# Kernel tuning notes

Measured on AMD Instinct MI355X. Metric: run time of the kernel, lower is better.

## Reference

```python
import jax, jax.numpy as jnp
import numpy as np

EPS = 1e-08
DIM = 256


def setup_inputs() -> dict:
    key = jax.random.key(0)
    k1, k2, k3 = jax.random.split(key, 3)
    B, S, D = 4, 4096, DIM
    x = jax.random.normal(k1, (B, S, D), dtype=jnp.float32)
    mask = jnp.ones((B, S), dtype=bool)
    # params of nn.Linear(dim, dim) and log_temp = log(0.1)
    bound = 1.0 / np.sqrt(D)
    W_v = jax.random.uniform(k2, (D, D), minval=-bound, maxval=bound, dtype=jnp.float32)
    b_v = jax.random.uniform(k3, (D,), minval=-bound, maxval=bound, dtype=jnp.float32)
    log_temp = jnp.log(jnp.asarray(0.1, dtype=jnp.float32))
    return {"x": x, "W_v": W_v, "b_v": b_v, "log_temp": log_temp, "mask": mask}


def reference(x, W_v, b_v, log_temp, mask):
    # temperature = exp(log_temp).clamp_min(1e-5)
    temp = jnp.maximum(jnp.exp(log_temp), 1e-5).astype(x.dtype)
    # squared pairwise euclidean distances (cdist^2), clamped to >= 0
    sq = jnp.sum(x * x, axis=-1)  # [B, S]
    d2 = sq[:, :, None] + sq[:, None, :] - 2.0 * jnp.einsum('bsd,btd->bst', x, x)
    d2 = jnp.maximum(d2, 0.0)  # [B, S, S]
    # Cauchy kernel: 1 / (1 + (dist/temp)^2)
    kernel = 1.0 / (1.0 + d2 / (temp * temp))
    valid = (mask[:, None, :] & mask[:, :, None]).astype(kernel.dtype)
    kernel = kernel * valid
    # row-normalize
    attn = kernel / jnp.maximum(jnp.sum(kernel, axis=-1, keepdims=True), EPS)
    v = x @ W_v.T + b_v  # [B, S, D]
    out = jnp.einsum('bst,btd->bsd', attn, v)
    return out
```

## Files before the change

### kernel.cpp

```cpp
#include <hip/hip_runtime.h>
#include <hip/hip_bf16.h>

#define S 4096
#define D 256
#define NB 4

typedef __attribute__((ext_vector_type(8))) __bf16 bf16x8;
typedef __attribute__((ext_vector_type(8))) short s16x8;
typedef __attribute__((ext_vector_type(4))) short s16x4;
typedef __attribute__((ext_vector_type(4))) float f32x4;
typedef __attribute__((ext_vector_type(8))) _Float16 h16x8;

#define MFMA(a, b, c) __builtin_amdgcn_mfma_f32_16x16x32_bf16(a, b, c, 0, 0, 0)
#define MFMA8(a, b, c) __builtin_amdgcn_mfma_f32_16x16x32_fp8_fp8(a, b, c, 0, 0, 0)

__device__ __forceinline__ short f2bf(float f) {
    union { float f; unsigned u; } v; v.f = f;
    unsigned r = v.u + 0x7fffu + ((v.u >> 16) & 1u);
    return (short)(r >> 16);
}

__device__ __forceinline__ short f2bf_hw(float f) {
    __bf16 h = (__bf16)f;
    return __builtin_bit_cast(short, h);
}

__device__ __forceinline__ void g2lds16(const char* g, char* l) {
    __builtin_amdgcn_global_load_lds(
        (const __attribute__((address_space(1))) unsigned int*)g,
        (__attribute__((address_space(3))) unsigned int*)l, 16, 0, 0);
}

__global__ __launch_bounds__(256) void k_prep(const float* __restrict__ x,
                                              const float* __restrict__ Wv,
                                              unsigned char* __restrict__ xb8,
                                              short* __restrict__ xt,
                                              short* __restrict__ wb,
                                              float* __restrict__ sqg) {
    const int tid = threadIdx.x;
    if (blockIdx.x >= 512) {
        int idx = (((int)blockIdx.x - 512) * 256 + tid) * 16;
        #pragma unroll
        for (int h = 0; h < 2; h++) {
            float4 f0 = *(const float4*)(Wv + idx + h * 8);
            float4 f1 = *(const float4*)(Wv + idx + h * 8 + 4);
            s16x8 o;
            o[0] = f2bf(f0.x); o[1] = f2bf(f0.y); o[2] = f2bf(f0.z); o[3] = f2bf(f0.w);
            o[4] = f2bf(f1.x); o[5] = f2bf(f1.y); o[6] = f2bf(f1.z); o[7] = f2bf(f1.w);
            *(s16x8*)(wb + idx + h * 8) = o;
        }
        return;
    }

    __shared__ short sX[32 * 264];
    const int b = blockIdx.x >> 7, s0 = (blockIdx.x & 127) * 32;
    const int row = tid >> 3, c8 = tid & 7;
    {
        const float* src = x + (size_t)(b * S + s0 + row) * D + c8 * 32;
        unsigned char* xrow = xb8 + (size_t)(b * S + s0 + row) * D;
        float ss = 0.f;
        int p8[8];
        #pragma unroll
        for (int j = 0; j < 8; j++) {
            float4 v = ((const float4*)src)[j];
            ss += v.x * v.x + v.y * v.y + v.z * v.z + v.w * v.w;
            s16x4 o;
            o.x = f2bf(v.x); o.y = f2bf(v.y); o.z = f2bf(v.z); o.w = f2bf(v.w);
            *(s16x4*)(sX + row * 264 + c8 * 32 + j * 4) = o;
            int pk = __builtin_amdgcn_cvt_pk_fp8_f32(v.x, v.y, 0, false);
            p8[j] = __builtin_amdgcn_cvt_pk_fp8_f32(v.z, v.w, pk, true);
        }
        ss += __shfl_xor(ss, 1, 64);
        ss += __shfl_xor(ss, 2, 64);
        ss += __shfl_xor(ss, 4, 64);
        int4 lo = {p8[0], p8[1], p8[2], p8[3]};
        int4 hi = {p8[4], p8[5], p8[6], p8[7]};
        *(int4*)(xrow + (((2 * c8) ^ (row & 7)) << 4)) = lo;
        *(int4*)(xrow + (((2 * c8 + 1) ^ (row & 7)) << 4)) = hi;
        if (c8 == 0) sqg[b * S + s0 + row] = ss;
    }
    __syncthreads();
    {
        short tmp[32];
        #pragma unroll
        for (int s = 0; s < 32; s++) tmp[s] = sX[s * 264 + tid];
        short* dst = xt + (size_t)(b * D + tid) * S + s0;
        #pragma unroll
        for (int i = 0; i < 4; i++)
            *(s16x8*)(dst + i * 8) = *(const s16x8*)(tmp + i * 8);
    }
}

template <int TSPLIT>
__global__ __launch_bounds__(256) void k_attn(const unsigned char* __restrict__ xb8,
                                              const short* __restrict__ xt,
                                              const float* __restrict__ sq,
                                              const float* __restrict__ logt,
                                              _Float16* __restrict__ pex,
                                              float* __restrict__ rws) {
    __shared__ char sXt[2][32 * 256];
    __shared__ short sK[2][64 * 36];
    __shared__ float sRow[64];

    const int tid = threadIdx.x;
    const int w = tid >> 6, lane = tid & 63;
    const int col = lane & 15, quad = lane >> 4;
    const int cx = col & 7;

    constexpr int LT = (TSPLIT == 4) ? 2 : 1;
    const int th = blockIdx.x & (TSPLIT - 1);
    const int b  = (blockIdx.x >> LT) & 3;
    const int qt = blockIdx.x >> (LT + 2);
    const int q0 = qt * 64;
    const int t_base = th * (S / TSPLIT);
    const int NT = (S / TSPLIT) / 32;

    float temp = fmaxf(__expf(logt[0]), 1e-5f);
    float t2 = temp * temp;
    float t2inv = __builtin_amdgcn_rcpf(t2);

    const unsigned char* xtb = xb8 + (size_t)b * S * D;
    const short* vtb = xt + (size_t)b * D * S;
    const float* sqb = sq + b * S;

    long xq[8];
    {
        const unsigned char* xrow = xtb + (size_t)(q0 + w * 16 + col) * D;
        #pragma unroll
        for (int ks = 0; ks < 8; ks++)
            xq[ks] = *(const long*)(xrow + (((ks * 2 + (quad >> 1)) ^ cx) << 4) + (quad & 1) * 8);
    }
    float sqq[4];
    #pragma unroll
    for (int rr = 0; rr < 4; rr++)
        sqq[rr] = sqb[q0 + w * 16 + quad * 4 + rr];

    f32x4 acc[4][4];
    #pragma unroll
    for (int mi = 0; mi < 4; mi++)
        #pragma unroll
        for (int ni = 0; ni < 4; ni++)
            acc[mi][ni] = (f32x4){0.f, 0.f, 0.f, 0.f};
    float rs[4] = {0.f, 0.f, 0.f, 0.f};

    {
        const char* g = (const char*)(xtb + (size_t)t_base * D);
        #pragma unroll
        for (int p = 0; p < 2; p++) {
            int c = p * 256 + tid;
            g2lds16(g + c * 16, &sXt[0][c * 16]);
        }
    }

    for (int i = 0; i < NT; i++) {
        const int t0 = t_base + i * 32;
        const int cur = i & 1;
        __syncthreads();

        if (i + 1 < NT) {
            const char* g = (const char*)(xtb + (size_t)(t0 + 32) * D);
            #pragma unroll
            for (int p = 0; p < 2; p++) {
                int c = p * 256 + tid;
                g2lds16(g + c * 16, &sXt[cur ^ 1][c * 16]);
            }
        }

        bf16x8 vb[4];
        if (i > 0) {
            const int tp = t0 - 32;
            #pragma unroll
            for (int ni = 0; ni < 4; ni++)
                vb[ni] = *(const bf16x8*)(vtb + (size_t)(w * 64 + ni * 16 + col) * S + tp + quad * 8);
        }
        float sqt0 = sqb[t0 + col], sqt1 = sqb[t0 + 16 + col];

        f32x4 p2v[2];
        p2v[0] = (f32x4){0.f, 0.f, 0.f, 0.f};
        p2v[1] = (f32x4){0.f, 0.f, 0.f, 0.f};
        #pragma unroll
        for (int ks = 0; ks < 8; ks++) {
            int co = (((ks * 2 + (quad >> 1)) ^ cx) << 4) + (quad & 1) * 8;
            long b0 = *(const long*)(&sXt[cur][col * 256 + co]);
            long b1 = *(const long*)(&sXt[cur][(col + 16) * 256 + co]);
            p2v[0] = MFMA8(xq[ks], b0, p2v[0]);
            p2v[1] = MFMA8(xq[ks], b1, p2v[1]);
        }

        const bool dg = ((unsigned)(t0 - q0) < 64u);
        const int rbase = w * 16 + quad * 4;
        #pragma unroll
        for (int t_ = 0; t_ < 2; t_++) {
            const float st = t2 + (t_ ? sqt1 : sqt0);
            if (dg) {
                const int tg = t0 + t_ * 16 + col;
                #pragma unroll
                for (int rr = 0; rr < 4; rr++) {
                    float d = fmaxf(st + sqq[rr] - 2.f * p2v[t_][rr], t2);
                    float u = __builtin_amdgcn_rcpf(d);
                    if (q0 + rbase + rr == tg) u = t2inv;
                    rs[rr] += u;
                    sK[cur][(rbase + rr) * 36 + t_ * 16 + col] = f2bf_hw(u);
                }
            } else {
                #pragma unroll
                for (int rr = 0; rr < 4; rr++) {
                    float d = fmaxf(st + sqq[rr] - 2.f * p2v[t_][rr], t2);
                    float u = __builtin_amdgcn_rcpf(d);
                    rs[rr] += u;
                    sK[cur][(rbase + rr) * 36 + t_ * 16 + col] = f2bf_hw(u);
                }
            }
        }

        if (i > 0) {
            #pragma unroll
            for (int mi = 0; mi < 4; mi++) {
                bf16x8 af = *(const bf16x8*)(&sK[cur ^ 1][(mi * 16 + col) * 36 + quad * 8]);
                #pragma unroll
                for (int ni = 0; ni < 4; ni++)
                    acc[mi][ni] = MFMA(af, vb[ni], acc[mi][ni]);
            }
        }
    }

    __syncthreads();
    {
        const int tp = t_base + (NT - 1) * 32;
        const int cur = (NT - 1) & 1;
        bf16x8 vb[4];
        #pragma unroll
        for (int ni = 0; ni < 4; ni++)
            vb[ni] = *(const bf16x8*)(vtb + (size_t)(w * 64 + ni * 16 + col) * S + tp + quad * 8);
        #pragma unroll
        for (int mi = 0; mi < 4; mi++) {
            bf16x8 af = *(const bf16x8*)(&sK[cur][(mi * 16 + col) * 36 + quad * 8]);
            #pragma unroll
            for (int ni = 0; ni < 4; ni++)
                acc[mi][ni] = MFMA(af, vb[ni], acc[mi][ni]);
        }
    }

    #pragma unroll
    for (int rr = 0; rr < 4; rr++) {
        float v = rs[rr];
        v += __shfl_xor(v, 1, 64);
        v += __shfl_xor(v, 2, 64);
        v += __shfl_xor(v, 4, 64);
        v += __shfl_xor(v, 8, 64);
        if (col == 0) sRow[w * 16 + quad * 4 + rr] = v;
    }
    __syncthreads();

    if (tid < 64) rws[(size_t)th * NB * S + b * S + q0 + tid] = sRow[tid];
    _Float16* ob = pex + (size_t)th * NB * S * D + (size_t)(b * S + q0) * D;
    #pragma unroll
    for (int mi = 0; mi < 4; mi++)
        #pragma unroll
        for (int rr = 0; rr < 4; rr++)
            #pragma unroll
            for (int ni = 0; ni < 4; ni++)
                ob[(size_t)(mi * 16 + quad * 4 + rr) * D + w * 64 + ni * 16 + col] =
                    (_Float16)acc[mi][ni][rr];
}

template <int NP>
__global__ __launch_bounds__(256) void k_post(const _Float16* __restrict__ pex,
                                              const float* __restrict__ rws,
                                              const short* __restrict__ wb,
                                              const float* __restrict__ bv,
                                              float* __restrict__ out) {
    __shared__ short sY[32 * 264];

    const int tid = threadIdx.x;
    const int w = tid >> 6, lane = tid & 63;
    const int col = lane & 15, quad = lane >> 4;
    const int b = blockIdx.x >> 7, s0 = (blockIdx.x & 127) * 32;

    bf16x8 wf[4][8];
    #pragma unroll
    for (int ni = 0; ni < 4; ni++)
        #pragma unroll
        for (int ks = 0; ks < 8; ks++)
            wf[ni][ks] = *(const bf16x8*)(wb + (size_t)(w * 64 + ni * 16 + col) * D + ks * 32 + quad * 8);

    {
        const int row = tid >> 3, c8 = tid & 7;
        const int gs = b * S + s0 + row;
        float rsum = rws[gs];
        #pragma unroll
        for (int p = 1; p < NP; p++) rsum += rws[(size_t)p * NB * S + gs];
        float rinv = __builtin_amdgcn_rcpf(fmaxf(rsum, 1e-8f));
        const _Float16* y0 = pex + (size_t)gs * D + c8 * 32;
        #pragma unroll
        for (int j = 0; j < 4; j++) {
            float f[8] = {0.f, 0.f, 0.f, 0.f, 0.f, 0.f, 0.f, 0.f};
            #pragma unroll
            for (int p = 0; p < NP; p++) {
                h16x8 a = *(const h16x8*)(y0 + (size_t)p * NB * S * D + j * 8);
                #pragma unroll
                for (int e = 0; e < 8; e++) f[e] += (float)a[e];
            }
            s16x8 o;
            #pragma unroll
            for (int e = 0; e < 8; e++) o[e] = f2bf_hw(f[e] * rinv);
            *(s16x8*)(sY + row * 264 + c8 * 32 + j * 8) = o;
        }
    }
    __syncthreads();

    f32x4 acc[2][4];
    #pragma unroll
    for (int mi = 0; mi < 2; mi++)
        #pragma unroll
        for (int ni = 0; ni < 4; ni++)
            acc[mi][ni] = (f32x4){0.f, 0.f, 0.f, 0.f};

    #pragma unroll
    for (int ks = 0; ks < 8; ks++) {
        bf16x8 a[2];
        #pragma unroll
        for (int mi = 0; mi < 2; mi++)
            a[mi] = *(const bf16x8*)(sY + (mi * 16 + col) * 264 + ks * 32 + quad * 8);
        #pragma unroll
        for (int mi = 0; mi < 2; mi++)
            #pragma unroll
            for (int ni = 0; ni < 4; ni++)
                acc[mi][ni] = MFMA(a[mi], wf[ni][ks], acc[mi][ni]);
    }

    float* ob = out + (size_t)(b * S + s0) * D;
    #pragma unroll
    for (int ni = 0; ni < 4; ni++) {
        int d = w * 64 + ni * 16 + col;
        float bvv = bv[d];
        #pragma unroll
        for (int mi = 0; mi < 2; mi++)
            #pragma unroll
            for (int r = 0; r < 4; r++)
                ob[(size_t)(mi * 16 + quad * 4 + r) * D + d] = acc[mi][ni][r] + bvv;
    }
}

extern "C" void kernel_launch(void* const* d_in, const int* in_sizes, int n_in,
                              void* d_out, int out_size, void* d_ws, size_t ws_size,
                              hipStream_t stream) {
    const float* x    = (const float*)d_in[0];
    const float* Wv   = (const float*)d_in[1];
    const float* bv   = (const float*)d_in[2];
    const float* logt = (const float*)d_in[3];
    float* out = (float*)d_out;

    char* ws = (char*)d_ws;
    unsigned char* xb8 = (unsigned char*)ws;
    short* xt  = (short*)(ws + 4194304);
    short* wb  = (short*)(ws + 12582912);
    float* sq  = (float*)(ws + 12713984);
    float* rws = (float*)(ws + 12779520);
    _Float16* pex = (_Float16*)(ws + 13041664);

    k_prep<<<528, 256, 0, stream>>>(x, Wv, xb8, xt, wb, sq);

    const size_t need4 = 13041664ull + 4ull * NB * S * D * 2;
    if (ws_size >= need4) {
        k_attn<4><<<NB * (S / 64) * 4, 256, 0, stream>>>(xb8, xt, sq, logt, pex, rws);
        k_post<4><<<NB * (S / 32), 256, 0, stream>>>(pex, rws, wb, bv, out);
    } else {
        k_attn<2><<<NB * (S / 64) * 2, 256, 0, stream>>>(xb8, xt, sq, logt, pex, rws);
        k_post<2><<<NB * (S / 32), 256, 0, stream>>>(pex, rws, wb, bv, out);
    }
}
```

Before: 188.7 us.

## Transpose distance MFMA operands, vectorize kernel-tile stores, reorder PV before kernel compute

Swaps the A/B operands of the fp8 distance MFMA so each lane holds four key columns for one query row. This lets the per-row sum live in a single register, reduced with two cross-quad shuffles instead of an LDS round-trip and barrier. The kernel values are packed into 4-wide bf16 stores to LDS, and the sq loads become vector loads. It also moves the P·V MFMA ahead of the elementwise kernel computation, raises its wave priority with s_setprio, and sets launch bounds to 3 blocks per CU, which may increase register pressure or spills.

```diff
diff --git a/kernel.cpp b/kernel.cpp
--- a/kernel.cpp
+++ b/kernel.cpp
@@ -92,15 +92,14 @@
 }
 
 template <int TSPLIT>
-__global__ __launch_bounds__(256) void k_attn(const unsigned char* __restrict__ xb8,
-                                              const short* __restrict__ xt,
-                                              const float* __restrict__ sq,
-                                              const float* __restrict__ logt,
-                                              _Float16* __restrict__ pex,
-                                              float* __restrict__ rws) {
+__global__ __launch_bounds__(256, 3) void k_attn(const unsigned char* __restrict__ xb8,
+                                                 const short* __restrict__ xt,
+                                                 const float* __restrict__ sq,
+                                                 const float* __restrict__ logt,
+                                                 _Float16* __restrict__ pex,
+                                                 float* __restrict__ rws) {
     __shared__ char sXt[2][32 * 256];
     __shared__ short sK[2][64 * 36];
-    __shared__ float sRow[64];
 
     const int tid = threadIdx.x;
     const int w = tid >> 6, lane = tid & 63;
@@ -130,10 +129,8 @@
         for (int ks = 0; ks < 8; ks++)
             xq[ks] = *(const long*)(xrow + (((ks * 2 + (quad >> 1)) ^ cx) << 4) + (quad & 1) * 8);
     }
-    float sqq[4];
-    #pragma unroll
-    for (int rr = 0; rr < 4; rr++)
-        sqq[rr] = sqb[q0 + w * 16 + quad * 4 + rr];
+    const int gq = q0 + w * 16 + col;
+    const float stq = sqb[gq] + t2;
 
     f32x4 acc[4][4];
     #pragma unroll
@@ -141,7 +138,7 @@
         #pragma unroll
         for (int ni = 0; ni < 4; ni++)
             acc[mi][ni] = (f32x4){0.f, 0.f, 0.f, 0.f};
-    float rs[4] = {0.f, 0.f, 0.f, 0.f};
+    float rs = 0.f;
 
     {
         const char* g = (const char*)(xtb + (size_t)t_base * D);
@@ -173,7 +170,6 @@
             for (int ni = 0; ni < 4; ni++)
                 vb[ni] = *(const bf16x8*)(vtb + (size_t)(w * 64 + ni * 16 + col) * S + tp + quad * 8);
         }
-        float sqt0 = sqb[t0 + col], sqt1 = sqb[t0 + 16 + col];
 
         f32x4 p2v[2];
         p2v[0] = (f32x4){0.f, 0.f, 0.f, 0.f};
@@ -181,39 +177,14 @@
         #pragma unroll
         for (int ks = 0; ks < 8; ks++) {
             int co = (((ks * 2 + (quad >> 1)) ^ cx) << 4) + (quad & 1) * 8;
-            long b0 = *(const long*)(&sXt[cur][col * 256 + co]);
-            long b1 = *(const long*)(&sXt[cur][(col + 16) * 256 + co]);
-            p2v[0] = MFMA8(xq[ks], b0, p2v[0]);
-            p2v[1] = MFMA8(xq[ks], b1, p2v[1]);
-        }
-
-        const bool dg = ((unsigned)(t0 - q0) < 64u);
-        const int rbase = w * 16 + quad * 4;
-        #pragma unroll
-        for (int t_ = 0; t_ < 2; t_++) {
-            const float st = t2 + (t_ ? sqt1 : sqt0);
-            if (dg) {
-                const int tg = t0 + t_ * 16 + col;
-                #pragma unroll
-                for (int rr = 0; rr < 4; rr++) {
-                    float d = fmaxf(st + sqq[rr] - 2.f * p2v[t_][rr], t2);
-                    float u = __builtin_amdgcn_rcpf(d);
-                    if (q0 + rbase + rr == tg) u = t2inv;
-                    rs[rr] += u;
-                    sK[cur][(rbase + rr) * 36 + t_ * 16 + col] = f2bf_hw(u);
-                }
-            } else {
-                #pragma unroll
-                for (int rr = 0; rr < 4; rr++) {
-                    float d = fmaxf(st + sqq[rr] - 2.f * p2v[t_][rr], t2);
-                    float u = __builtin_amdgcn_rcpf(d);
-                    rs[rr] += u;
-                    sK[cur][(rbase + rr) * 36 + t_ * 16 + col] = f2bf_hw(u);
-                }
-            }
+            long a0 = *(const long*)(&sXt[cur][col * 256 + co]);
+            long a1 = *(const long*)(&sXt[cur][(col + 16) * 256 + co]);
+            p2v[0] = MFMA8(a0, xq[ks], p2v[0]);
+            p2v[1] = MFMA8(a1, xq[ks], p2v[1]);
         }
 
         if (i > 0) {
+            __builtin_amdgcn_s_setprio(1);
             #pragma unroll
             for (int mi = 0; mi < 4; mi++) {
                 bf16x8 af = *(const bf16x8*)(&sK[cur ^ 1][(mi * 16 + col) * 36 + quad * 8]);
@@ -221,6 +192,38 @@
                 for (int ni = 0; ni < 4; ni++)
                     acc[mi][ni] = MFMA(af, vb[ni], acc[mi][ni]);
             }
+            __builtin_amdgcn_s_setprio(0);
+        }
+
+        {
+            f32x4 sqt0 = *(const f32x4*)(sqb + t0 + quad * 4);
+            f32x4 sqt1 = *(const f32x4*)(sqb + t0 + 16 + quad * 4);
+            const bool dg = ((unsigned)(t0 - q0) < 64u);
+            const int qmt = gq - t0;
+            #pragma unroll
+            for (int tf = 0; tf < 2; tf++) {
+                f32x4 sqt = tf ? sqt1 : sqt0;
+                s16x4 pk;
+                if (dg) {
+                    #pragma unroll
+                    for (int rr = 0; rr < 4; rr++) {
+                        float d = fmaxf(stq + sqt[rr] - 2.f * p2v[tf][rr], t2);
+                        float u = __builtin_amdgcn_rcpf(d);
+                        if (qmt == tf * 16 + quad * 4 + rr) u = t2inv;
+                        rs += u;
+                        pk[rr] = f2bf_hw(u);
+                    }
+                } else {
+                    #pragma unroll
+                    for (int rr = 0; rr < 4; rr++) {
+                        float d = fmaxf(stq + sqt[rr] - 2.f * p2v[tf][rr], t2);
+                        float u = __builtin_amdgcn_rcpf(d);
+                        rs += u;
+                        pk[rr] = f2bf_hw(u);
+                    }
+                }
+                *(s16x4*)(&sK[cur][(w * 16 + col) * 36 + tf * 16 + quad * 4]) = pk;
+            }
         }
     }
 
@@ -241,18 +244,10 @@
         }
     }
 
-    #pragma unroll
-    for (int rr = 0; rr < 4; rr++) {
-        float v = rs[rr];
-        v += __shfl_xor(v, 1, 64);
-        v += __shfl_xor(v, 2, 64);
-        v += __shfl_xor(v, 4, 64);
-        v += __shfl_xor(v, 8, 64);
-        if (col == 0) sRow[w * 16 + quad * 4 + rr] = v;
-    }
-    __syncthreads();
-
-    if (tid < 64) rws[(size_t)th * NB * S + b * S + q0 + tid] = sRow[tid];
+    rs += __shfl_xor(rs, 16, 64);
+    rs += __shfl_xor(rs, 32, 64);
+    if (quad == 0) rws[(size_t)th * NB * S + b * S + gq] = rs;
+
     _Float16* ob = pex + (size_t)th * NB * S * D + (size_t)(b * S + q0) * D;
     #pragma unroll
     for (int mi = 0; mi < 4; mi++)
```

New measurement: 223.7 us. 18.6% more time.

## Load key tiles directly into registers and reorder attention loop schedule

Applied to the files above, without the earlier changes.

Drops the LDS staging of fp8 key tiles and has each lane load its MFMA B operands straight from global memory into double-buffered register arrays, prefetched one iteration ahead. The distance MFMAs are split into two independent accumulator chains. The PV MFMAs now run before the Cauchy kernel computation and are given raised wave priority, and a manual barrier replaces __syncthreads. The launch is also fixed to the TSPLIT=2 variant. Together these aim to cut LDS traffic and barrier stalls and to overlap the two GEMMs, at the cost of more VGPRs and redundant global loads, since each wave now fetches the same key rows.

```diff
diff --git a/kernel.cpp b/kernel.cpp
--- a/kernel.cpp
+++ b/kernel.cpp
@@ -23,12 +23,6 @@
 __device__ __forceinline__ short f2bf_hw(float f) {
     __bf16 h = (__bf16)f;
     return __builtin_bit_cast(short, h);
-}
-
-__device__ __forceinline__ void g2lds16(const char* g, char* l) {
-    __builtin_amdgcn_global_load_lds(
-        (const __attribute__((address_space(1))) unsigned int*)g,
-        (__attribute__((address_space(3))) unsigned int*)l, 16, 0, 0);
 }
 
 __global__ __launch_bounds__(256) void k_prep(const float* __restrict__ x,
@@ -98,7 +92,6 @@
                                               const float* __restrict__ logt,
                                               _Float16* __restrict__ pex,
                                               float* __restrict__ rws) {
-    __shared__ char sXt[2][32 * 256];
     __shared__ short sK[2][64 * 36];
     __shared__ float sRow[64];
 
@@ -123,12 +116,17 @@
     const short* vtb = xt + (size_t)b * D * S;
     const float* sqb = sq + b * S;
 
+    int ofs[8];
+    #pragma unroll
+    for (int ks = 0; ks < 8; ks++)
+        ofs[ks] = (((ks * 2 + (quad >> 1)) ^ cx) << 4) + (quad & 1) * 8;
+
     long xq[8];
     {
         const unsigned char* xrow = xtb + (size_t)(q0 + w * 16 + col) * D;
         #pragma unroll
         for (int ks = 0; ks < 8; ks++)
-            xq[ks] = *(const long*)(xrow + (((ks * 2 + (quad >> 1)) ^ cx) << 4) + (quad & 1) * 8);
+            xq[ks] = *(const long*)(xrow + ofs[ks]);
     }
     float sqq[4];
     #pragma unroll
@@ -143,88 +141,104 @@
             acc[mi][ni] = (f32x4){0.f, 0.f, 0.f, 0.f};
     float rs[4] = {0.f, 0.f, 0.f, 0.f};
 
-    {
-        const char* g = (const char*)(xtb + (size_t)t_base * D);
-        #pragma unroll
-        for (int p = 0; p < 2; p++) {
-            int c = p * 256 + tid;
-            g2lds16(g + c * 16, &sXt[0][c * 16]);
-        }
-    }
-
-    for (int i = 0; i < NT; i++) {
-        const int t0 = t_base + i * 32;
-        const int cur = i & 1;
-        __syncthreads();
-
-        if (i + 1 < NT) {
-            const char* g = (const char*)(xtb + (size_t)(t0 + 32) * D);
-            #pragma unroll
-            for (int p = 0; p < 2; p++) {
-                int c = p * 256 + tid;
-                g2lds16(g + c * 16, &sXt[cur ^ 1][c * 16]);
-            }
-        }
-
-        bf16x8 vb[4];
-        if (i > 0) {
-            const int tp = t0 - 32;
-            #pragma unroll
-            for (int ni = 0; ni < 4; ni++)
-                vb[ni] = *(const bf16x8*)(vtb + (size_t)(w * 64 + ni * 16 + col) * S + tp + quad * 8);
-        }
-        float sqt0 = sqb[t0 + col], sqt1 = sqb[t0 + 16 + col];
-
-        f32x4 p2v[2];
-        p2v[0] = (f32x4){0.f, 0.f, 0.f, 0.f};
-        p2v[1] = (f32x4){0.f, 0.f, 0.f, 0.f};
-        #pragma unroll
-        for (int ks = 0; ks < 8; ks++) {
-            int co = (((ks * 2 + (quad >> 1)) ^ cx) << 4) + (quad & 1) * 8;
-            long b0 = *(const long*)(&sXt[cur][col * 256 + co]);
-            long b1 = *(const long*)(&sXt[cur][(col + 16) * 256 + co]);
-            p2v[0] = MFMA8(xq[ks], b0, p2v[0]);
-            p2v[1] = MFMA8(xq[ks], b1, p2v[1]);
-        }
-
-        const bool dg = ((unsigned)(t0 - q0) < 64u);
-        const int rbase = w * 16 + quad * 4;
-        #pragma unroll
-        for (int t_ = 0; t_ < 2; t_++) {
-            const float st = t2 + (t_ ? sqt1 : sqt0);
-            if (dg) {
-                const int tg = t0 + t_ * 16 + col;
-                #pragma unroll
-                for (int rr = 0; rr < 4; rr++) {
-                    float d = fmaxf(st + sqq[rr] - 2.f * p2v[t_][rr], t2);
-                    float u = __builtin_amdgcn_rcpf(d);
-                    if (q0 + rbase + rr == tg) u = t2inv;
-                    rs[rr] += u;
-                    sK[cur][(rbase + rr) * 36 + t_ * 16 + col] = f2bf_hw(u);
-                }
-            } else {
-                #pragma unroll
-                for (int rr = 0; rr < 4; rr++) {
-                    float d = fmaxf(st + sqq[rr] - 2.f * p2v[t_][rr], t2);
-                    float u = __builtin_amdgcn_rcpf(d);
-                    rs[rr] += u;
-                    sK[cur][(rbase + rr) * 36 + t_ * 16 + col] = f2bf_hw(u);
-                }
-            }
-        }
-
-        if (i > 0) {
-            #pragma unroll
-            for (int mi = 0; mi < 4; mi++) {
-                bf16x8 af = *(const bf16x8*)(&sK[cur ^ 1][(mi * 16 + col) * 36 + quad * 8]);
-                #pragma unroll
-                for (int ni = 0; ni < 4; ni++)
-                    acc[mi][ni] = MFMA(af, vb[ni], acc[mi][ni]);
-            }
-        }
-    }
-
-    __syncthreads();
+    const unsigned char* ar0 = xtb + (size_t)(t_base + col) * D;
+    const unsigned char* ar1 = ar0 + 16 * D;
+
+    long BbA[16], BbB[16];
+    #pragma unroll
+    for (int ks = 0; ks < 8; ks++) {
+        BbA[2 * ks]     = *(const long*)(ar0 + ofs[ks]);
+        BbA[2 * ks + 1] = *(const long*)(ar1 + ofs[ks]);
+    }
+    ar0 += 32 * D; ar1 += 32 * D;
+
+#define ITER_BODY(i, Bc, Bn)                                                          \
+    {                                                                                 \
+        const int t0 = t_base + (i) * 32;                                             \
+        const int cur = (i) & 1;                                                      \
+              \
+        if ((i) + 1 < NT) {                                                           \
+            _Pragma("unroll")                                                         \
+            for (int ks = 0; ks < 8; ks++) {                                          \
+                Bn[2 * ks]     = *(const long*)(ar0 + ofs[ks]);                       \
+                Bn[2 * ks + 1] = *(const long*)(ar1 + ofs[ks]);                       \
+            }                                                                         \
+            ar0 += 32 * D; ar1 += 32 * D;                                             \
+        }                                                                             \
+                                \
+        bf16x8 vb[4];                                                                 \
+        if ((i) > 0) {                                                                \
+            const int tp = t0 - 32;                                                   \
+            _Pragma("unroll")                                                         \
+            for (int ni = 0; ni < 4; ni++)                                            \
+                vb[ni] = *(const bf16x8*)(vtb + (size_t)(w * 64 + ni * 16 + col) * S  \
+                                          + tp + quad * 8);                           \
+        }                                                                             \
+             \
+        f32x4 pa0 = (f32x4){0.f,0.f,0.f,0.f}, pa1 = (f32x4){0.f,0.f,0.f,0.f};         \
+        f32x4 pb0 = (f32x4){0.f,0.f,0.f,0.f}, pb1 = (f32x4){0.f,0.f,0.f,0.f};         \
+        _Pragma("unroll")                                                             \
+        for (int ks = 0; ks < 4; ks++) {                                              \
+            pa0 = MFMA8(xq[ks],     Bc[2 * ks],     pa0);                             \
+            pa1 = MFMA8(xq[ks],     Bc[2 * ks + 1], pa1);                             \
+            pb0 = MFMA8(xq[ks + 4], Bc[2 * ks + 8], pb0);                             \
+            pb1 = MFMA8(xq[ks + 4], Bc[2 * ks + 9], pb1);                             \
+        }                                                                             \
+                                         \
+        if ((i) > 0) {                                                                \
+            __builtin_amdgcn_s_setprio(1);                                            \
+            _Pragma("unroll")                                                         \
+            for (int mi = 0; mi < 4; mi++) {                                          \
+                bf16x8 af = *(const bf16x8*)(&sK[cur ^ 1][(mi * 16 + col) * 36        \
+                                                          + quad * 8]);               \
+                _Pragma("unroll")                                                     \
+                for (int ni = 0; ni < 4; ni++)                                        \
+                    acc[mi][ni] = MFMA(af, vb[ni], acc[mi][ni]);                      \
+            }                                                                         \
+            __builtin_amdgcn_s_setprio(0);                                            \
+        }                                                                             \
+                                            \
+        {                                                                             \
+            f32x4 p2v[2]; p2v[0] = pa0 + pb0; p2v[1] = pa1 + pb1;                     \
+            float sqt0 = sqb[t0 + col], sqt1 = sqb[t0 + 16 + col];                    \
+            const bool dg = ((unsigned)(t0 - q0) < 64u);                              \
+            const int rbase = w * 16 + quad * 4;                                      \
+            _Pragma("unroll")                                                         \
+            for (int tf = 0; tf < 2; tf++) {                                          \
+                const float st = t2 + (tf ? sqt1 : sqt0);                             \
+                if (dg) {                                                             \
+                    const int tg = t0 + tf * 16 + col;                                \
+                    _Pragma("unroll")                                                 \
+                    for (int rr = 0; rr < 4; rr++) {                                  \
+                        float d = fmaxf(st + sqq[rr] - 2.f * p2v[tf][rr], t2);        \
+                        float u = __builtin_amdgcn_rcpf(d);                           \
+                        if (q0 + rbase + rr == tg) u = t2inv;                         \
+                        rs[rr] += u;                                                  \
+                        sK[cur][(rbase + rr) * 36 + tf * 16 + col] = f2bf_hw(u);      \
+                    }                                                                 \
+                } else {                                                              \
+                    _Pragma("unroll")                                                 \
+                    for (int rr = 0; rr < 4; rr++) {                                  \
+                        float d = fmaxf(st + sqq[rr] - 2.f * p2v[tf][rr], t2);        \
+                        float u = __builtin_amdgcn_rcpf(d);                           \
+                        rs[rr] += u;                                                  \
+                        sK[cur][(rbase + rr) * 36 + tf * 16 + col] = f2bf_hw(u);      \
+                    }                                                                 \
+                }                                                                     \
+            }                                                                         \
+        }                                                                             \
+                \
+        asm volatile("s_waitcnt lgkmcnt(0)" ::: "memory");                            \
+        __builtin_amdgcn_s_barrier();                                                 \
+        __builtin_amdgcn_sched_barrier(0);                                            \
+    }
+
+    for (int ii = 0; ii < NT; ii += 2) {
+        ITER_BODY(ii,     BbA, BbB)
+        ITER_BODY(ii + 1, BbB, BbA)
+    }
+#undef ITER_BODY
+
     {
         const int tp = t_base + (NT - 1) * 32;
         const int cur = (NT - 1) & 1;
@@ -360,13 +374,6 @@
     _Float16* pex = (_Float16*)(ws + 13041664);
 
     k_prep<<<528, 256, 0, stream>>>(x, Wv, xb8, xt, wb, sq);
-
-    const size_t need4 = 13041664ull + 4ull * NB * S * D * 2;
-    if (ws_size >= need4) {
-        k_attn<4><<<NB * (S / 64) * 4, 256, 0, stream>>>(xb8, xt, sq, logt, pex, rws);
-        k_post<4><<<NB * (S / 32), 256, 0, stream>>>(pex, rws, wb, bv, out);
-    } else {
-        k_attn<2><<<NB * (S / 64) * 2, 256, 0, stream>>>(xb8, xt, sq, logt, pex, rws);
-        k_post<2><<<NB * (S / 32), 256, 0, stream>>>(pex, rws, wb, bv, out);
-    }
-}
+    k_attn<2><<<NB * (S / 64) * 2, 256, 0, stream>>>(xb8, xt, sq, logt, pex, rws);
+    k_post<2><<<NB * (S / 32), 256, 0, stream>>>(pex, rws, wb, bv, out);
+}
```

Result: slower. 321.2 us (+70.2%).
